# Kernel optimization log

Hardware: AMD Instinct MI355X
Metric: run time of the kernel (lower is better)

Reference implementation:

```python
import jax, jax.numpy as jnp
import numpy as np
from functools import partial

STEPLIM = 10
TOL = 1e-4


def _knn1(pc1, pc2):
    """1-NN of each point in pc1 (B,N1,3) against pc2 (B,N2,3).
    Same math as torch: L2 norm of broadcasted diff, topk(k=1, smallest),
    expressed via the |a|^2+|b|^2-2ab expansion to avoid the (B,N1,N2,3) diff."""
    sq1 = jnp.sum(pc1 * pc1, axis=-1)                       # (B,N1)
    sq2 = jnp.sum(pc2 * pc2, axis=-1)                       # (B,N2)
    cross = jnp.einsum('bnd,bmd->bnm', pc1, pc2)            # (B,N1,N2)
    d2 = jnp.maximum(sq1[..., :, None] + sq2[..., None, :] - 2.0 * cross, 0.0)
    idx = jnp.argmin(d2, axis=-1)                           # (B,N1)
    dmin = jnp.sqrt(jnp.take_along_axis(d2, idx[..., None], axis=-1)[..., 0])
    return dmin, idx


def _points_transform(pts1, pts2):
    """Kabsch/SVD rigid fit: R, t such that R @ pts1 + t ~= pts2 (EPnP._points_transform)."""
    c1 = jnp.mean(pts1, axis=-2, keepdims=True)             # (B,1,3)
    c2 = jnp.mean(pts2, axis=-2, keepdims=True)
    q1 = pts1 - c1
    q2 = pts2 - c2
    H = jnp.einsum('bni,bnj->bij', q1, q2)                  # (B,3,3) covariance
    U, S, Vh = jnp.linalg.svd(H)
    V = jnp.swapaxes(Vh, -1, -2)
    d = jnp.sign(jnp.linalg.det(jnp.einsum('bik,bjk->bij', V, U)))  # det(V U^T)
    sgn = jnp.stack([jnp.ones_like(d), jnp.ones_like(d), d], axis=-1)  # fix reflection
    R = jnp.einsum('bik,bk,bjk->bij', V, sgn, U)            # V diag(1,1,d) U^T
    t = c2 - jnp.einsum('bij,bnj->bni', R, c1)              # (B,1,3)
    return R, t


def _apply(R, t, pts):
    return jnp.einsum('bij,bnj->bni', R, pts) + t


def _icp(p1, p2):
    B = p1.shape[0]

    def step(carry, _):
        temppc, err, done = carry
        dmin, idx = _knn1(temppc, p2)
        errnew = jnp.mean(dmin, axis=-1)                    # (B,)
        # torch: first iteration err is None -> no break check; err0=inf makes cond False (nan < tol)
        cond = jnp.all(jnp.abs((errnew - err) / err) < TOL)
        new_done = done | cond
        matched = jax.vmap(lambda pc, i: pc[i])(p2, idx)    # (B,N1,3) gather of p2
        R, t = _points_transform(temppc, matched)
        temppc_new = _apply(R, t, temppc)
        temppc = jnp.where(new_done, temppc, temppc_new)
        err = jnp.where(new_done, err, errnew)
        return (temppc, err, new_done), None

    err0 = jnp.full((B,), jnp.inf, dtype=p1.dtype)
    done0 = jnp.array(False)
    (temppc, _, _), _ = jax.lax.scan(step, (p1, err0, done0), None, length=STEPLIM + 1)
    R, t = _points_transform(p1, temppc)
    return jnp.concatenate([R, jnp.swapaxes(t, -1, -2)], axis=-1)  # (B,3,4) = [R | t]


def setup_inputs() -> dict:
    key = jax.random.key(0)
    k1, k2 = jax.random.split(key)
    p1 = jax.random.normal(k1, (1, 8192, 3), dtype=jnp.float32)
    p2 = jax.random.normal(k2, (1, 8192, 3), dtype=jnp.float32)
    return {"p1": p1, "p2": p2}


def reference(p1, p2):
    return _icp(p1, p2)
```

## Files before the change

### kernel.cpp

```cpp
#include <hip/hip_runtime.h>
#include <float.h>
#include <math.h>

#define N_PTS 8192
#define NB    256
#define NT    512
#define QPB   32
#define NRG   32
#define RC    256
#define STEPS 11
#define TOLV  1e-4

#define PADSLOT(i) ((i) + ((i) >> 6))
#define SC_SZ (N_PTS + N_PTS/64)

#define WS_P2F    0
#define WS_TEMPPC 131072
#define WS_BPA    229376
#define WS_BPB    262144
#define WS_ERRH   294912
#define WS_DONEH  295040

__device__ void kabsch3(const double H[3][3], const double c1[3], const double c2[3],
                        double R[3][3], double t[3]) {
    double A[3][3];
    for (int i = 0; i < 3; ++i)
        for (int j = 0; j < 3; ++j) {
            double sacc = 0.0;
            for (int k = 0; k < 3; ++k) sacc += H[k][i] * H[k][j];
            A[i][j] = sacc;
        }
    double V[3][3] = {{1,0,0},{0,1,0},{0,0,1}};
    for (int sweep = 0; sweep < 6; ++sweep) {
        const int PQ[3][2] = {{0,1},{0,2},{1,2}};
        for (int mm = 0; mm < 3; ++mm) {
            int p = PQ[mm][0], q = PQ[mm][1];
            double apq = A[p][q];
            if (fabs(apq) < 1e-300) continue;
            double app = A[p][p], aqq = A[q][q];
            double tau = (aqq - app) / (2.0 * apq);
            double tt = (tau >= 0.0) ? 1.0 / (tau + sqrt(1.0 + tau*tau))
                                     : 1.0 / (tau - sqrt(1.0 + tau*tau));
            double c = 1.0 / sqrt(1.0 + tt*tt), s = tt * c;
            A[p][p] = app - tt * apq;
            A[q][q] = aqq + tt * apq;
            A[p][q] = 0.0; A[q][p] = 0.0;
            int k = 3 - p - q;
            double akp = A[k][p], akq = A[k][q];
            A[k][p] = c*akp - s*akq; A[p][k] = A[k][p];
            A[k][q] = s*akp + c*akq; A[q][k] = A[k][q];
            for (int r = 0; r < 3; ++r) {
                double vp = V[r][p], vq = V[r][q];
                V[r][p] = c*vp - s*vq;
                V[r][q] = s*vp + c*vq;
            }
        }
    }
    double lam[3] = {A[0][0], A[1][1], A[2][2]};
    int ord[3] = {0,1,2};
    for (int i = 0; i < 2; ++i)
        for (int j = i+1; j < 3; ++j)
            if (lam[ord[j]] > lam[ord[i]]) { int tmp = ord[i]; ord[i] = ord[j]; ord[j] = tmp; }
    double v0[3] = {V[0][ord[0]], V[1][ord[0]], V[2][ord[0]]};
    double v1[3] = {V[0][ord[1]], V[1][ord[1]], V[2][ord[1]]};
    double v2[3] = {V[0][ord[2]], V[1][ord[2]], V[2][ord[2]]};

    double u0[3], u1[3], hv2[3];
    for (int i = 0; i < 3; ++i) u0[i] = H[i][0]*v0[0] + H[i][1]*v0[1] + H[i][2]*v0[2];
    double n0 = sqrt(u0[0]*u0[0] + u0[1]*u0[1] + u0[2]*u0[2]);
    n0 = fmax(n0, 1e-300);
    for (int i = 0; i < 3; ++i) u0[i] /= n0;

    for (int i = 0; i < 3; ++i) u1[i] = H[i][0]*v1[0] + H[i][1]*v1[1] + H[i][2]*v1[2];
    double d01 = u1[0]*u0[0] + u1[1]*u0[1] + u1[2]*u0[2];
    for (int i = 0; i < 3; ++i) u1[i] -= d01 * u0[i];
    double n1 = sqrt(u1[0]*u1[0] + u1[1]*u1[1] + u1[2]*u1[2]);
    n1 = fmax(n1, 1e-300);
    for (int i = 0; i < 3; ++i) u1[i] /= n1;

    double u2[3] = {u0[1]*u1[2] - u0[2]*u1[1],
                    u0[2]*u1[0] - u0[0]*u1[2],
                    u0[0]*u1[1] - u0[1]*u1[0]};
    for (int i = 0; i < 3; ++i) hv2[i] = H[i][0]*v2[0] + H[i][1]*v2[1] + H[i][2]*v2[2];
    if (hv2[0]*u2[0] + hv2[1]*u2[1] + hv2[2]*u2[2] < 0.0) {
        v2[0] = -v2[0]; v2[1] = -v2[1]; v2[2] = -v2[2];
    }
    double cx = v1[1]*v2[2] - v1[2]*v2[1];
    double cy = v1[2]*v2[0] - v1[0]*v2[2];
    double cz = v1[0]*v2[1] - v1[1]*v2[0];
    double detV = v0[0]*cx + v0[1]*cy + v0[2]*cz;
    double dsg = (detV < 0.0) ? -1.0 : 1.0;

    for (int i = 0; i < 3; ++i)
        for (int j = 0; j < 3; ++j)
            R[i][j] = v0[i]*u0[j] + v1[i]*u1[j] + dsg * v2[i]*u2[j];
    for (int i = 0; i < 3; ++i)
        t[i] = c2[i] - (R[i][0]*c1[0] + R[i][1]*c1[1] + R[i][2]*c1[2]);
}

__device__ __forceinline__ void build_H(const double s[16], double c1[3], double c2[3],
                                        double H[3][3]) {
    const double Nn = (double)N_PTS;
    c1[0] = s[1]/Nn; c1[1] = s[2]/Nn; c1[2] = s[3]/Nn;
    c2[0] = s[4]/Nn; c2[1] = s[5]/Nn; c2[2] = s[6]/Nn;
    for (int i = 0; i < 3; ++i)
        for (int j = 0; j < 3; ++j)
            H[i][j] = s[7 + 3*i + j] - Nn * c1[i] * c2[j];
}

__global__ __launch_bounds__(NT, 2) void icp_step(
    const float* __restrict__ p1, const float* __restrict__ p2,
    float4* __restrict__ p2f, float* __restrict__ temppc,
    const double* __restrict__ bp_prev, double* __restrict__ bp_cur,
    double* __restrict__ err_hist, int* __restrict__ done_hist, int it)
{
    __shared__ float4 sCand[SC_SZ];
    __shared__ float4 sQ[QPB];
    __shared__ float  sWB[8][16][2];
    __shared__ int    sWI[8][16][2];
    __shared__ float  sRt[12];
    __shared__ int    sDone;
    const int tid = threadIdx.x, bid = blockIdx.x;

    const int latched = (it > 0) ? done_hist[it-1] : 0;
    const bool scan_possible = (it < STEPS) && !latched;

    if (scan_possible) {
        if (it == 0) {
            #pragma unroll
            for (int k = 0; k < 16; ++k) {
                int i = tid + NT*k;
                float x = p2[3*i], y = p2[3*i+1], z = p2[3*i+2];
                sCand[PADSLOT(i)] = make_float4(x, y, z, x*x + y*y + z*z);
            }
        } else {
            #pragma unroll
            for (int k = 0; k < 16; ++k) {
                int i = tid + NT*k;
                sCand[PADSLOT(i)] = p2f[i];
            }
        }
    }

    int done = 0;
    if (it == 0) {
        __syncthreads();
        if (bid == 0 && tid == 0) { err_hist[0] = __builtin_inf(); done_hist[0] = 0; }
        if (tid < QPB) {
            int i = bid*QPB + tid;
            p2f[i] = sCand[PADSLOT(i)];
        }
    } else if (latched) {
        done = 1;
        if (bid == 0 && tid == 0) { done_hist[it] = 1; err_hist[it] = err_hist[it-1]; }
    } else {
        if (tid < 64) {
            double sv[16];
            #pragma unroll
            for (int k = 0; k < 16; ++k) sv[k] = 0.0;
            #pragma unroll
            for (int jj = 0; jj < 4; ++jj) {
                const double* row = bp_prev + (tid + 64*jj)*16;
                #pragma unroll
                for (int k = 0; k < 16; ++k) sv[k] += row[k];
            }
            #pragma unroll
            for (int off = 1; off < 64; off <<= 1) {
                #pragma unroll
                for (int k = 0; k < 16; ++k) sv[k] += __shfl_xor(sv[k], off, 64);
            }
            if (tid == 0) {
                double errnew = sv[0] / (double)N_PTS;
                double err = err_hist[it-1];
                double rel = fabs((errnew - err) / err);
                int nd = (rel < TOLV) ? 1 : 0;
                if (bid == 0) { done_hist[it] = nd; err_hist[it] = nd ? err : errnew; }
                sDone = nd;
                if (!nd) {
                    double c1[3], c2[3], H[3][3], Rm[3][3], tv[3];
                    build_H(sv, c1, c2, H);
                    kabsch3(H, c1, c2, Rm, tv);
                    for (int i = 0; i < 3; ++i) {
                        sRt[3*i]   = (float)Rm[i][0];
                        sRt[3*i+1] = (float)Rm[i][1];
                        sRt[3*i+2] = (float)Rm[i][2];
                        sRt[9+i]   = (float)tv[i];
                    }
                }
            }
        }
        __syncthreads();
        done = sDone;
    }

    if (done && it < STEPS) return;

    if (tid < QPB) {
        int q = bid*QPB + tid;
        float x, y, z;
        if (it == 0) {
            x = p1[3*q]; y = p1[3*q+1]; z = p1[3*q+2];
            temppc[3*q] = x; temppc[3*q+1] = y; temppc[3*q+2] = z;
        } else {
            x = temppc[3*q]; y = temppc[3*q+1]; z = temppc[3*q+2];
            if (!done) {
                float nx = fmaf(sRt[0], x, fmaf(sRt[1], y, fmaf(sRt[2], z, sRt[9])));
                float ny = fmaf(sRt[3], x, fmaf(sRt[4], y, fmaf(sRt[5], z, sRt[10])));
                float nz = fmaf(sRt[6], x, fmaf(sRt[7], y, fmaf(sRt[8], z, sRt[11])));
                x = nx; y = ny; z = nz;
                temppc[3*q] = x; temppc[3*q+1] = y; temppc[3*q+2] = z;
            }
        }
        sQ[tid] = make_float4(x, y, z, x*x + y*y + z*z);
    }
    __syncthreads();

    if (it == STEPS) {
        if (tid < 64) {
            double vals[16];
            if (tid < 32) {
                int q = bid*QPB + tid;
                float ax = p1[3*q], ay = p1[3*q+1], az = p1[3*q+2];
                float4 b4 = sQ[tid];
                vals[0] = 0.0;
                vals[1] = (double)ax;   vals[2] = (double)ay;   vals[3] = (double)az;
                vals[4] = (double)b4.x; vals[5] = (double)b4.y; vals[6] = (double)b4.z;
                vals[7]  = (double)ax*b4.x; vals[8]  = (double)ax*b4.y; vals[9]  = (double)ax*b4.z;
                vals[10] = (double)ay*b4.x; vals[11] = (double)ay*b4.y; vals[12] = (double)ay*b4.z;
                vals[13] = (double)az*b4.x; vals[14] = (double)az*b4.y; vals[15] = (double)az*b4.z;
            } else {
                #pragma unroll
                for (int k = 0; k < 16; ++k) vals[k] = 0.0;
            }
            #pragma unroll
            for (int off = 1; off < 32; off <<= 1) {
                #pragma unroll
                for (int k = 0; k < 16; ++k) vals[k] += __shfl_xor(vals[k], off, 64);
            }
            if (tid == 0) {
                double* d = bp_cur + bid*16;
                #pragma unroll
                for (int k = 0; k < 16; ++k) d[k] = vals[k];
            }
        }
        return;
    }

    const int pr = tid & 15;
    const int r  = tid >> 4;
    const float4 qa = sQ[2*pr], qb = sQ[2*pr+1];
    const float ax0 = -2.f*qa.x, ay0 = -2.f*qa.y, az0 = -2.f*qa.z;
    const float ax1 = -2.f*qb.x, ay1 = -2.f*qb.y, az1 = -2.f*qb.z;
    float best0 = FLT_MAX, best1 = FLT_MAX;
    int   bi0 = 0, bi1 = 0;
    const int sb0 = r * 260;
    const int gb0 = r * 256;

    for (int jo = 0; jo < 4; ++jo) {
        const int sb = sb0 + jo*65;
        const int gB = gb0 + jo*64;
        #pragma unroll 8
        for (int j = 0; j < 64; ++j) {
            float4 sj = sCand[sb + j];
            int idx = gB + j;
            float v0 = fmaf(ax0, sj.x, sj.w); v0 = fmaf(ay0, sj.y, v0); v0 = fmaf(az0, sj.z, v0);
            if (v0 < best0) { best0 = v0; bi0 = idx; }
            float v1 = fmaf(ax1, sj.x, sj.w); v1 = fmaf(ay1, sj.y, v1); v1 = fmaf(az1, sj.z, v1);
            if (v1 < best1) { best1 = v1; bi1 = idx; }
        }
    }

    #pragma unroll
    for (int off = 16; off <= 32; off <<= 1) {
        float ov0 = __shfl_xor(best0, off, 64); int oi0 = __shfl_xor(bi0, off, 64);
        if (ov0 < best0 || (ov0 == best0 && oi0 < bi0)) { best0 = ov0; bi0 = oi0; }
        float ov1 = __shfl_xor(best1, off, 64); int oi1 = __shfl_xor(bi1, off, 64);
        if (ov1 < best1 || (ov1 == best1 && oi1 < bi1)) { best1 = ov1; bi1 = oi1; }
    }
    const int w = tid >> 6;
    if ((tid & 63) < 16) {
        sWB[w][pr][0] = best0; sWI[w][pr][0] = bi0;
        sWB[w][pr][1] = best1; sWI[w][pr][1] = bi1;
    }
    __syncthreads();

    if (tid < 64) {
        double vals[16];
        if (tid < 32) {
            int mm = tid >> 1, wh = tid & 1;
            float bv = sWB[0][mm][wh]; int bi = sWI[0][mm][wh];
            #pragma unroll
            for (int ww = 1; ww < 8; ++ww) {
                float ov = sWB[ww][mm][wh]; int oi = sWI[ww][mm][wh];
                if (ov < bv || (ov == bv && oi < bi)) { bv = ov; bi = oi; }
            }
            float4 a4 = sQ[tid];
            float d2 = fmaxf(bv + a4.w, 0.0f);
            float dmin = sqrtf(d2);
            float4 b4 = p2f[bi];
            vals[0] = (double)dmin;
            vals[1] = (double)a4.x; vals[2] = (double)a4.y; vals[3] = (double)a4.z;
            vals[4] = (double)b4.x; vals[5] = (double)b4.y; vals[6] = (double)b4.z;
            vals[7]  = (double)a4.x*b4.x; vals[8]  = (double)a4.x*b4.y; vals[9]  = (double)a4.x*b4.z;
            vals[10] = (double)a4.y*b4.x; vals[11] = (double)a4.y*b4.y; vals[12] = (double)a4.y*b4.z;
            vals[13] = (double)a4.z*b4.x; vals[14] = (double)a4.z*b4.y; vals[15] = (double)a4.z*b4.z;
        } else {
            #pragma unroll
            for (int k = 0; k < 16; ++k) vals[k] = 0.0;
        }
        #pragma unroll
        for (int off = 1; off < 32; off <<= 1) {
            #pragma unroll
            for (int k = 0; k < 16; ++k) vals[k] += __shfl_xor(vals[k], off, 64);
        }
        if (tid == 0) {
            double* d = bp_cur + bid*16;
            #pragma unroll
            for (int k = 0; k < 16; ++k) d[k] = vals[k];
        }
    }
}

__global__ void icp_final(const double* __restrict__ bp, float* __restrict__ out) {
    int tid = threadIdx.x;
    double sv[16];
    #pragma unroll
    for (int k = 0; k < 16; ++k) sv[k] = 0.0;
    #pragma unroll
    for (int j = 0; j < 4; ++j) {
        const double* row = bp + (tid + 64*j)*16;
        #pragma unroll
        for (int k = 0; k < 16; ++k) sv[k] += row[k];
    }
    #pragma unroll
    for (int off = 1; off < 64; off <<= 1) {
        #pragma unroll
        for (int k = 0; k < 16; ++k) sv[k] += __shfl_xor(sv[k], off, 64);
    }
    if (tid == 0) {
        double c1[3], c2[3], H[3][3], Rm[3][3], tv[3];
        build_H(sv, c1, c2, H);
        kabsch3(H, c1, c2, Rm, tv);
        for (int i = 0; i < 3; ++i) {
            out[4*i + 0] = (float)Rm[i][0];
            out[4*i + 1] = (float)Rm[i][1];
            out[4*i + 2] = (float)Rm[i][2];
            out[4*i + 3] = (float)tv[i];
        }
    }
}

extern "C" void kernel_launch(void* const* d_in, const int* in_sizes, int n_in,
                              void* d_out, int out_size, void* d_ws, size_t ws_size,
                              hipStream_t stream) {
    const float* p1 = (const float*)d_in[0];
    const float* p2 = (const float*)d_in[1];
    float* out = (float*)d_out;
    char* ws = (char*)d_ws;

    float4* p2f       = (float4*)(ws + WS_P2F);
    float*  temppc    = (float*) (ws + WS_TEMPPC);
    double* bpA       = (double*)(ws + WS_BPA);
    double* bpB       = (double*)(ws + WS_BPB);
    double* err_hist  = (double*)(ws + WS_ERRH);
    int*    done_hist = (int*)   (ws + WS_DONEH);

    for (int it = 0; it <= STEPS; ++it) {
        double* cur  = (it & 1) ? bpB : bpA;
        double* prev = (it & 1) ? bpA : bpB;
        icp_step<<<NB, NT, 0, stream>>>(p1, p2, p2f, temppc, prev, cur,
                                        err_hist, done_hist, it);
    }
    icp_final<<<1, 64, 0, stream>>>(bpB, out);
}
```

Baseline: 293.7 us.

## Register-block eight queries per thread in the nearest-neighbour scan

```diff
diff --git a/kernel.cpp b/kernel.cpp
--- a/kernel.cpp
+++ b/kernel.cpp
@@ -6,8 +6,9 @@
 #define NB    256
 #define NT    512
 #define QPB   32
-#define NRG   32
-#define RC    256
+#define QPT   8
+#define NRG   128
+#define RC    64
 #define STEPS 11
 #define TOLV  1e-4
 
@@ -116,8 +117,8 @@
 {
     __shared__ float4 sCand[SC_SZ];
     __shared__ float4 sQ[QPB];
-    __shared__ float  sWB[8][16][2];
-    __shared__ int    sWI[8][16][2];
+    __shared__ float  sWB[8][QPT];
+    __shared__ int    sWI[8][QPT];
     __shared__ float  sRt[12];
     __shared__ int    sDone;
     const int tid = threadIdx.x, bid = blockIdx.x;
@@ -246,58 +247,70 @@
         return;
     }
 
-    const int pr = tid & 15;
-    const int r  = tid >> 4;
-    const float4 qa = sQ[2*pr], qb = sQ[2*pr+1];
-    const float ax0 = -2.f*qa.x, ay0 = -2.f*qa.y, az0 = -2.f*qa.z;
-    const float ax1 = -2.f*qb.x, ay1 = -2.f*qb.y, az1 = -2.f*qb.z;
-    float best0 = FLT_MAX, best1 = FLT_MAX;
-    int   bi0 = 0, bi1 = 0;
-    const int sb0 = r * 260;
-    const int gb0 = r * 256;
-
-    for (int jo = 0; jo < 4; ++jo) {
-        const int sb = sb0 + jo*65;
-        const int gB = gb0 + jo*64;
-        #pragma unroll 8
-        for (int j = 0; j < 64; ++j) {
-            float4 sj = sCand[sb + j];
-            int idx = gB + j;
-            float v0 = fmaf(ax0, sj.x, sj.w); v0 = fmaf(ay0, sj.y, v0); v0 = fmaf(az0, sj.z, v0);
-            if (v0 < best0) { best0 = v0; bi0 = idx; }
-            float v1 = fmaf(ax1, sj.x, sj.w); v1 = fmaf(ay1, sj.y, v1); v1 = fmaf(az1, sj.z, v1);
-            if (v1 < best1) { best1 = v1; bi1 = idx; }
-        }
-    }
-
-    #pragma unroll
-    for (int off = 16; off <= 32; off <<= 1) {
-        float ov0 = __shfl_xor(best0, off, 64); int oi0 = __shfl_xor(bi0, off, 64);
-        if (ov0 < best0 || (ov0 == best0 && oi0 < bi0)) { best0 = ov0; bi0 = oi0; }
-        float ov1 = __shfl_xor(best1, off, 64); int oi1 = __shfl_xor(bi1, off, 64);
-        if (ov1 < best1 || (ov1 == best1 && oi1 < bi1)) { best1 = ov1; bi1 = oi1; }
+    const int g = tid >> 7;
+    const int r = tid & 127;
+    float qx[QPT], qy[QPT], qz[QPT];
+    #pragma unroll
+    for (int k = 0; k < QPT; ++k) {
+        float4 a = sQ[QPT*g + k];
+        qx[k] = -2.f*a.x; qy[k] = -2.f*a.y; qz[k] = -2.f*a.z;
+    }
+    float best[QPT]; int bi[QPT];
+    #pragma unroll
+    for (int k = 0; k < QPT; ++k) { best[k] = FLT_MAX; bi[k] = 0; }
+
+    const int sb = 65*r;
+    const int gb = 64*r;
+
+#define PROC8(SJ, JJ)                                                 \
+    {                                                                 \
+        _Pragma("unroll")                                             \
+        for (int k = 0; k < QPT; ++k) {                               \
+            float v = fmaf(qx[k], (SJ).x, (SJ).w);                    \
+            v = fmaf(qy[k], (SJ).y, v);                               \
+            v = fmaf(qz[k], (SJ).z, v);                               \
+            if (v < best[k]) { best[k] = v; bi[k] = (JJ); }           \
+        }                                                             \
+    }
+
+    float4 cur = sCand[sb];
+    #pragma unroll 4
+    for (int j = 0; j < RC - 1; ++j) {
+        float4 nxt = sCand[sb + j + 1];
+        PROC8(cur, gb + j);
+        cur = nxt;
+    }
+    PROC8(cur, gb + RC - 1);
+#undef PROC8
+
+    #pragma unroll
+    for (int off = 1; off < 64; off <<= 1) {
+        #pragma unroll
+        for (int k = 0; k < QPT; ++k) {
+            float ov = __shfl_xor(best[k], off, 64);
+            int   oi = __shfl_xor(bi[k],  off, 64);
+            if (ov < best[k] || (ov == best[k] && oi < bi[k])) { best[k] = ov; bi[k] = oi; }
+        }
     }
     const int w = tid >> 6;
-    if ((tid & 63) < 16) {
-        sWB[w][pr][0] = best0; sWI[w][pr][0] = bi0;
-        sWB[w][pr][1] = best1; sWI[w][pr][1] = bi1;
+    if ((tid & 63) == 0) {
+        #pragma unroll
+        for (int k = 0; k < QPT; ++k) { sWB[w][k] = best[k]; sWI[w][k] = bi[k]; }
     }
     __syncthreads();
 
     if (tid < 64) {
         double vals[16];
         if (tid < 32) {
-            int mm = tid >> 1, wh = tid & 1;
-            float bv = sWB[0][mm][wh]; int bi = sWI[0][mm][wh];
-            #pragma unroll
-            for (int ww = 1; ww < 8; ++ww) {
-                float ov = sWB[ww][mm][wh]; int oi = sWI[ww][mm][wh];
-                if (ov < bv || (ov == bv && oi < bi)) { bv = ov; bi = oi; }
-            }
-            float4 a4 = sQ[tid];
+            int q = tid;
+            int gg = q >> 3, k = q & 7;
+            float bv = sWB[2*gg][k];   int bix = sWI[2*gg][k];
+            float ov = sWB[2*gg+1][k]; int oi  = sWI[2*gg+1][k];
+            if (ov < bv || (ov == bv && oi < bix)) { bv = ov; bix = oi; }
+            float4 a4 = sQ[q];
             float d2 = fmaxf(bv + a4.w, 0.0f);
             float dmin = sqrtf(d2);
-            float4 b4 = p2f[bi];
+            float4 b4 = p2f[bix];
             vals[0] = (double)dmin;
             vals[1] = (double)a4.x; vals[2] = (double)a4.y; vals[3] = (double)a4.z;
             vals[4] = (double)b4.x; vals[5] = (double)b4.y; vals[6] = (double)b4.z;
```

Measured after the change: 305.5 us. +4.0%, slower.
